# Kernel tuning notes

Measured on AMD Instinct MI355X. Metric: run time of the kernel, lower is better.

The kernel has to match this reference:

```python
import jax, jax.numpy as jnp
import numpy as np

EPS = 1e-12  # tf.nn.l2_normalize epsilon
ALPHA = 0.9  # hard-negative threshold factor (function default)


def l2_normalize(x):
    # matches tf.nn.l2_normalize: x / sqrt(max(sum(x^2), eps))
    return x * jax.lax.rsqrt(jnp.maximum(jnp.sum(x * x, axis=-1, keepdims=True), EPS))


def setup_inputs() -> dict:
    key = jax.random.key(0)
    k1, k2, k3, k4, k5 = jax.random.split(key, 5)
    B, N, K, D, C = 16, 8, 2048, 512, 11
    return {
        "predicted_vectors": jax.random.normal(k1, (B, C, D), dtype=jnp.float32),
        "positive_vectors": jax.random.normal(k2, (B, N, D), dtype=jnp.float32),
        "negative_gallery": jax.random.normal(k3, (B, N, K, D), dtype=jnp.float32),
        "cluster_centers": jax.random.normal(k4, (C, D), dtype=jnp.float32),
        "positive_categories": jax.random.randint(k5, (B, N), 0, 12, dtype=jnp.int32),
    }


def reference(predicted_vectors, positive_vectors, negative_gallery, cluster_centers, positive_categories):
    # center-base combined contrastive loss (IQON3000, categories 1-11)
    cat_idx = jnp.clip(positive_categories - 1, 0, 10)                 # (B, N)
    # gather predicted slot per category: (B, N, D)
    pred_sel = jnp.take_along_axis(predicted_vectors, cat_idx[..., None], axis=1)
    centers = cluster_centers[cat_idx]                                  # (B, N, D)
    pred_norm = l2_normalize(pred_sel - centers)                        # (B, N, D)
    pos_norm = l2_normalize(positive_vectors - centers)                 # (B, N, D)
    neg_norm = l2_normalize(negative_gallery - centers[:, :, None, :])  # (B, N, K, D)

    sim_pos = jnp.sum(pred_norm * pos_norm, axis=-1)                    # (B, N)
    sim_neg = jnp.einsum('bnd,bnkd->bnk', pred_norm, neg_norm)          # (B, N, K)

    thresh = ALPHA * sim_pos[..., None]
    hard_mask = (sim_neg - sim_pos[..., None] >= thresh).astype(jnp.float32)

    exp_pos = jnp.exp(sim_pos)                                          # sims bounded in [-1,1]
    neg_sum = jnp.sum(jnp.exp(sim_neg) * hard_mask, axis=-1)
    denom = jnp.maximum(exp_pos + neg_sum, 1e-7)
    loss = -jnp.log(exp_pos / denom)
    return jnp.mean(loss)
```

## Files before the change

### kernel.cpp

```cpp
#include <hip/hip_runtime.h>
#include <math.h>

#define BB 16
#define NN 8
#define KK 2048
#define DD 512
#define CC 11
#define BN (BB*NN)
#define NCHUNK 16
#define KCHUNK (KK/NCHUNK)
#define EPSN 1e-12f
#define ALPHA 0.9f

struct f8 { float v[8]; };

__device__ __forceinline__ f8 load8(const float* base, int l) {
    const float4* p = (const float4*)base;
    float4 x = p[l];
    float4 y = p[l + 64];
    f8 r;
    r.v[0] = x.x; r.v[1] = x.y; r.v[2] = x.z; r.v[3] = x.w;
    r.v[4] = y.x; r.v[5] = y.y; r.v[6] = y.z; r.v[7] = y.w;
    return r;
}

__device__ __forceinline__ float wave_reduce64(float v) {
    #pragma unroll
    for (int off = 1; off < 64; off <<= 1)
        v += __shfl_xor(v, off, 64);
    return v;
}

__device__ __forceinline__ int clamp_cat(int c) {
    c = c - 1;
    return c < 0 ? 0 : (c > 10 ? 10 : c);
}

__global__ __launch_bounds__(64)
void k1_simpos(const float* __restrict__ pred, const float* __restrict__ pos,
               const float* __restrict__ centers, const int* __restrict__ cats,
               float* __restrict__ simpos) {
    int bn = blockIdx.x;
    int b  = bn / NN;
    int l  = threadIdx.x;
    int cat = clamp_cat(cats[bn]);

    f8 pr = load8(pred + ((size_t)b * CC + cat) * DD, l);
    f8 cc = load8(centers + (size_t)cat * DD, l);
    f8 po = load8(pos + (size_t)bn * DD, l);

    float ssa = 0.f, ssb = 0.f;
    float a[8], p[8];
    #pragma unroll
    for (int j = 0; j < 8; ++j) {
        a[j] = pr.v[j] - cc.v[j];
        p[j] = po.v[j] - cc.v[j];
        ssa += a[j] * a[j];
        ssb += p[j] * p[j];
    }
    ssa = wave_reduce64(ssa);
    ssb = wave_reduce64(ssb);
    float ia = 1.0f / sqrtf(fmaxf(ssa, EPSN));
    float ib = 1.0f / sqrtf(fmaxf(ssb, EPSN));

    float dp = 0.f;
    #pragma unroll
    for (int j = 0; j < 8; ++j)
        dp += (a[j] * ia) * (p[j] * ib);
    dp = wave_reduce64(dp);

    if (l == 0) simpos[bn] = dp;
}

__global__ __launch_bounds__(256)
void k2_neg(const float* __restrict__ pred, const float* __restrict__ neg,
            const float* __restrict__ centers, const int* __restrict__ cats,
            const float* __restrict__ simpos, float* __restrict__ partials) {
    int blk   = blockIdx.x;
    int bn    = blk / NCHUNK;
    int chunk = blk % NCHUNK;
    int b     = bn / NN;
    int wave  = threadIdx.x >> 6;
    int l     = threadIdx.x & 63;
    int g     = l >> 5;
    int sub   = l & 31;

    int cat = clamp_cat(cats[bn]);

    const float4* c4 = (const float4*)(centers + (size_t)cat * DD);
    const float4* p4 = (const float4*)(pred + ((size_t)b * CC + cat) * DD);

    float cc[16], pn[16];
    float ss = 0.f;
    #pragma unroll
    for (int j = 0; j < 4; ++j) {
        float4 cv = c4[sub + j * 32];
        float4 pv = p4[sub + j * 32];
        cc[j*4+0] = cv.x; cc[j*4+1] = cv.y; cc[j*4+2] = cv.z; cc[j*4+3] = cv.w;
        float d0 = pv.x - cv.x, d1 = pv.y - cv.y, d2 = pv.z - cv.z, d3 = pv.w - cv.w;
        pn[j*4+0] = d0; pn[j*4+1] = d1; pn[j*4+2] = d2; pn[j*4+3] = d3;
        ss += d0*d0 + d1*d1 + d2*d2 + d3*d3;
    }
    #pragma unroll
    for (int off = 1; off < 32; off <<= 1) ss += __shfl_xor(ss, off, 64);
    float inv = 1.0f / sqrtf(fmaxf(ss, EPSN));
    #pragma unroll
    for (int j = 0; j < 16; ++j) pn[j] *= inv;

    float sp = simpos[bn];
    float acc = 0.f;

    const float4* nb4 = (const float4*)(neg + ((size_t)bn * KK + (size_t)chunk * KCHUNK) * DD);
    const int V4 = DD / 4;

    float4 cur[4];
    {
        const float4* vb = nb4 + (size_t)(2 * wave + g) * V4;
        #pragma unroll
        for (int j = 0; j < 4; ++j) cur[j] = vb[sub + j * 32];
    }

    for (int it = 0; it < 16; ++it) {
        float4 nxt[4] = {cur[0], cur[1], cur[2], cur[3]};
        if (it + 1 < 16) {
            const float4* vb = nb4 + (size_t)(2 * (wave + 4 * (it + 1)) + g) * V4;
            #pragma unroll
            for (int j = 0; j < 4; ++j) nxt[j] = vb[sub + j * 32];
        }

        float ds = 0.f, s2 = 0.f;
        #pragma unroll
        for (int j = 0; j < 4; ++j) {
            float d;
            d = cur[j].x - cc[j*4+0]; ds += pn[j*4+0] * d; s2 += d * d;
            d = cur[j].y - cc[j*4+1]; ds += pn[j*4+1] * d; s2 += d * d;
            d = cur[j].z - cc[j*4+2]; ds += pn[j*4+2] * d; s2 += d * d;
            d = cur[j].w - cc[j*4+3]; ds += pn[j*4+3] * d; s2 += d * d;
        }
        #pragma unroll
        for (int off = 1; off < 32; off <<= 1) {
            ds += __shfl_xor(ds, off, 64);
            s2 += __shfl_xor(s2, off, 64);
        }
        float sn = ds * (1.0f / sqrtf(fmaxf(s2, EPSN)));
        if (sub == 0 && (sn - sp >= ALPHA * sp)) acc += expf(sn);

        #pragma unroll
        for (int j = 0; j < 4; ++j) cur[j] = nxt[j];
    }

    acc += __shfl_xor(acc, 32, 64);

    __shared__ float sacc[4];
    if (l == 0) sacc[wave] = acc;
    __syncthreads();
    if (threadIdx.x == 0)
        partials[blk] = sacc[0] + sacc[1] + sacc[2] + sacc[3];
}

__global__ __launch_bounds__(128)
void k3_final(const float* __restrict__ simpos, const float* __restrict__ partials,
              float* __restrict__ out) {
    int bn = threadIdx.x;
    float ns = 0.f;
    for (int i = 0; i < NCHUNK; ++i)
        ns += partials[bn * NCHUNK + i];
    float sp = simpos[bn];
    float ep = expf(sp);
    float denom = fmaxf(ep + ns, 1e-7f);
    float loss = -logf(ep / denom);

    __shared__ float s[BN];
    s[bn] = loss;
    __syncthreads();
    #pragma unroll
    for (int st = 64; st > 0; st >>= 1) {
        if (bn < st) s[bn] += s[bn + st];
        __syncthreads();
    }
    if (bn == 0) out[0] = s[0] / (float)BN;
}

extern "C" void kernel_launch(void* const* d_in, const int* in_sizes, int n_in,
                              void* d_out, int out_size, void* d_ws, size_t ws_size,
                              hipStream_t stream) {
    const float* pred    = (const float*)d_in[0];
    const float* pos     = (const float*)d_in[1];
    const float* neg     = (const float*)d_in[2];
    const float* centers = (const float*)d_in[3];
    const int*   cats    = (const int*)d_in[4];

    float* out = (float*)d_out;

    float* simpos   = (float*)d_ws;
    float* partials = simpos + BN;

    k1_simpos<<<BN, 64, 0, stream>>>(pred, pos, centers, cats, simpos);
    k2_neg<<<BN * NCHUNK, 256, 0, stream>>>(pred, neg, centers, cats, simpos, partials);
    k3_final<<<1, 128, 0, stream>>>(simpos, partials, out);
}
```

Baseline: 101.7 us.

## Fuse positive-similarity kernel into negative kernel and use nontemporal loads

Removes the separate sim_pos kernel by having every block of the negative kernel compute the positive similarity itself from pred, pos and centers, with chunk 0 writing it for the final kernel. This drops one launch and the dependency on a prior kernel, at the cost of redundant small reads per block. The negative gallery stream now uses nontemporal loads, and the prefetch loop is peeled so the last iteration has no conditional.

```diff
diff --git a/kernel.cpp b/kernel.cpp
--- a/kernel.cpp
+++ b/kernel.cpp
@@ -12,70 +12,18 @@
 #define EPSN 1e-12f
 #define ALPHA 0.9f
 
-struct f8 { float v[8]; };
-
-__device__ __forceinline__ f8 load8(const float* base, int l) {
-    const float4* p = (const float4*)base;
-    float4 x = p[l];
-    float4 y = p[l + 64];
-    f8 r;
-    r.v[0] = x.x; r.v[1] = x.y; r.v[2] = x.z; r.v[3] = x.w;
-    r.v[4] = y.x; r.v[5] = y.y; r.v[6] = y.z; r.v[7] = y.w;
-    return r;
-}
-
-__device__ __forceinline__ float wave_reduce64(float v) {
-    #pragma unroll
-    for (int off = 1; off < 64; off <<= 1)
-        v += __shfl_xor(v, off, 64);
-    return v;
-}
+typedef float fx4 __attribute__((ext_vector_type(4)));
 
 __device__ __forceinline__ int clamp_cat(int c) {
     c = c - 1;
     return c < 0 ? 0 : (c > 10 ? 10 : c);
 }
 
-__global__ __launch_bounds__(64)
-void k1_simpos(const float* __restrict__ pred, const float* __restrict__ pos,
-               const float* __restrict__ centers, const int* __restrict__ cats,
-               float* __restrict__ simpos) {
-    int bn = blockIdx.x;
-    int b  = bn / NN;
-    int l  = threadIdx.x;
-    int cat = clamp_cat(cats[bn]);
-
-    f8 pr = load8(pred + ((size_t)b * CC + cat) * DD, l);
-    f8 cc = load8(centers + (size_t)cat * DD, l);
-    f8 po = load8(pos + (size_t)bn * DD, l);
-
-    float ssa = 0.f, ssb = 0.f;
-    float a[8], p[8];
-    #pragma unroll
-    for (int j = 0; j < 8; ++j) {
-        a[j] = pr.v[j] - cc.v[j];
-        p[j] = po.v[j] - cc.v[j];
-        ssa += a[j] * a[j];
-        ssb += p[j] * p[j];
-    }
-    ssa = wave_reduce64(ssa);
-    ssb = wave_reduce64(ssb);
-    float ia = 1.0f / sqrtf(fmaxf(ssa, EPSN));
-    float ib = 1.0f / sqrtf(fmaxf(ssb, EPSN));
-
-    float dp = 0.f;
-    #pragma unroll
-    for (int j = 0; j < 8; ++j)
-        dp += (a[j] * ia) * (p[j] * ib);
-    dp = wave_reduce64(dp);
-
-    if (l == 0) simpos[bn] = dp;
-}
-
 __global__ __launch_bounds__(256)
-void k2_neg(const float* __restrict__ pred, const float* __restrict__ neg,
-            const float* __restrict__ centers, const int* __restrict__ cats,
-            const float* __restrict__ simpos, float* __restrict__ partials) {
+void k2_neg(const float* __restrict__ pred, const float* __restrict__ pos,
+            const float* __restrict__ neg, const float* __restrict__ centers,
+            const int* __restrict__ cats,
+            float* __restrict__ simpos, float* __restrict__ partials) {
     int blk   = blockIdx.x;
     int bn    = blk / NCHUNK;
     int chunk = blk % NCHUNK;
@@ -89,53 +37,59 @@
 
     const float4* c4 = (const float4*)(centers + (size_t)cat * DD);
     const float4* p4 = (const float4*)(pred + ((size_t)b * CC + cat) * DD);
+    const float4* q4 = (const float4*)(pos + (size_t)bn * DD);
 
     float cc[16], pn[16];
-    float ss = 0.f;
+    float ssa = 0.f, ssp = 0.f, dap = 0.f;
     #pragma unroll
     for (int j = 0; j < 4; ++j) {
         float4 cv = c4[sub + j * 32];
         float4 pv = p4[sub + j * 32];
+        float4 qv = q4[sub + j * 32];
         cc[j*4+0] = cv.x; cc[j*4+1] = cv.y; cc[j*4+2] = cv.z; cc[j*4+3] = cv.w;
-        float d0 = pv.x - cv.x, d1 = pv.y - cv.y, d2 = pv.z - cv.z, d3 = pv.w - cv.w;
-        pn[j*4+0] = d0; pn[j*4+1] = d1; pn[j*4+2] = d2; pn[j*4+3] = d3;
-        ss += d0*d0 + d1*d1 + d2*d2 + d3*d3;
+        float a0 = pv.x - cv.x, a1 = pv.y - cv.y, a2 = pv.z - cv.z, a3 = pv.w - cv.w;
+        float q0 = qv.x - cv.x, q1 = qv.y - cv.y, q2 = qv.z - cv.z, q3 = qv.w - cv.w;
+        pn[j*4+0] = a0; pn[j*4+1] = a1; pn[j*4+2] = a2; pn[j*4+3] = a3;
+        ssa += a0*a0 + a1*a1 + a2*a2 + a3*a3;
+        ssp += q0*q0 + q1*q1 + q2*q2 + q3*q3;
+        dap += a0*q0 + a1*q1 + a2*q2 + a3*q3;
     }
     #pragma unroll
-    for (int off = 1; off < 32; off <<= 1) ss += __shfl_xor(ss, off, 64);
-    float inv = 1.0f / sqrtf(fmaxf(ss, EPSN));
+    for (int off = 1; off < 32; off <<= 1) {
+        ssa += __shfl_xor(ssa, off, 64);
+        ssp += __shfl_xor(ssp, off, 64);
+        dap += __shfl_xor(dap, off, 64);
+    }
+    float ia = 1.0f / sqrtf(fmaxf(ssa, EPSN));
+    float ib = 1.0f / sqrtf(fmaxf(ssp, EPSN));
+    float sp = dap * ia * ib;
     #pragma unroll
-    for (int j = 0; j < 16; ++j) pn[j] *= inv;
+    for (int j = 0; j < 16; ++j) pn[j] *= ia;
 
-    float sp = simpos[bn];
+    if (chunk == 0 && threadIdx.x == 0) simpos[bn] = sp;
+
     float acc = 0.f;
 
-    const float4* nb4 = (const float4*)(neg + ((size_t)bn * KK + (size_t)chunk * KCHUNK) * DD);
+    const fx4* nb4 = (const fx4*)(neg + ((size_t)bn * KK + (size_t)chunk * KCHUNK) * DD);
     const int V4 = DD / 4;
 
-    float4 cur[4];
+    fx4 cur[4];
     {
-        const float4* vb = nb4 + (size_t)(2 * wave + g) * V4;
+        const fx4* vb = nb4 + (size_t)(2 * wave + g) * V4;
         #pragma unroll
-        for (int j = 0; j < 4; ++j) cur[j] = vb[sub + j * 32];
+        for (int j = 0; j < 4; ++j) cur[j] = __builtin_nontemporal_load(&vb[sub + j * 32]);
     }
 
-    for (int it = 0; it < 16; ++it) {
-        float4 nxt[4] = {cur[0], cur[1], cur[2], cur[3]};
-        if (it + 1 < 16) {
-            const float4* vb = nb4 + (size_t)(2 * (wave + 4 * (it + 1)) + g) * V4;
-            #pragma unroll
-            for (int j = 0; j < 4; ++j) nxt[j] = vb[sub + j * 32];
-        }
-
+    auto process = [&](const fx4* v) {
         float ds = 0.f, s2 = 0.f;
         #pragma unroll
         for (int j = 0; j < 4; ++j) {
-            float d;
-            d = cur[j].x - cc[j*4+0]; ds += pn[j*4+0] * d; s2 += d * d;
-            d = cur[j].y - cc[j*4+1]; ds += pn[j*4+1] * d; s2 += d * d;
-            d = cur[j].z - cc[j*4+2]; ds += pn[j*4+2] * d; s2 += d * d;
-            d = cur[j].w - cc[j*4+3]; ds += pn[j*4+3] * d; s2 += d * d;
+            #pragma unroll
+            for (int e = 0; e < 4; ++e) {
+                float d = v[j][e] - cc[j*4+e];
+                ds += pn[j*4+e] * d;
+                s2 += d * d;
+            }
         }
         #pragma unroll
         for (int off = 1; off < 32; off <<= 1) {
@@ -144,10 +98,20 @@
         }
         float sn = ds * (1.0f / sqrtf(fmaxf(s2, EPSN)));
         if (sub == 0 && (sn - sp >= ALPHA * sp)) acc += expf(sn);
+    };
+
+    for (int it = 0; it < 15; ++it) {
+        fx4 nxt[4];
+        const fx4* vb = nb4 + (size_t)(2 * (wave + 4 * (it + 1)) + g) * V4;
+        #pragma unroll
+        for (int j = 0; j < 4; ++j) nxt[j] = __builtin_nontemporal_load(&vb[sub + j * 32]);
+
+        process(cur);
 
         #pragma unroll
         for (int j = 0; j < 4; ++j) cur[j] = nxt[j];
     }
+    process(cur);
 
     acc += __shfl_xor(acc, 32, 64);
 
@@ -195,7 +159,6 @@
     float* simpos   = (float*)d_ws;
     float* partials = simpos + BN;
 
-    k1_simpos<<<BN, 64, 0, stream>>>(pred, pos, centers, cats, simpos);
-    k2_neg<<<BN * NCHUNK, 256, 0, stream>>>(pred, neg, centers, cats, simpos, partials);
+    k2_neg<<<BN * NCHUNK, 256, 0, stream>>>(pred, pos, neg, centers, cats, simpos, partials);
     k3_final<<<1, 128, 0, stream>>>(simpos, partials, out);
 }
```

Measured after the change: 91.63 us (median of 2 runs). -9.9%, faster.
